# Kernel tuning notes

Measured on AMD Instinct MI355X. Metric: run time of the kernel, lower is better.

The kernel has to match this reference:

```python
import jax, jax.numpy as jnp
import numpy as np

GROUP = 16          # c.MAX_GROUP_SIZE
NEG_SLOPE = 0.2     # GATConv default negative_slope
BN_EPS = 1e-5       # BatchNorm1d eps (eval mode, running stats (0,1))


def setup_inputs() -> dict:
    key = jax.random.key(0)
    ks = iter(jax.random.split(key, 64))
    N, E, F_IN = 8192, 262144, 1024
    d = {}
    d['x'] = jax.random.normal(next(ks), (N, F_IN), jnp.float32)
    d['edge_index'] = jax.random.randint(next(ks), (2, E), 0, N, dtype=jnp.int32)
    def p(shape, scale=0.05):
        return jax.random.normal(next(ks), shape, jnp.float32) * scale
    # GATConv params (heads=1): lin weight [in,out] (no bias), att_src/att_dst [out], bias [out]
    d['W1'], d['a1s'], d['a1d'], d['b1'] = p((F_IN, 128)), p((128,)), p((128,)), p((128,))
    d['W2'], d['a2s'], d['a2d'], d['b2'] = p((128, 256)), p((256,)), p((256,)), p((256,))
    d['W3'], d['a3s'], d['a3d'], d['b3'] = p((256, 128)), p((128,)), p((128,)), p((128,))
    # LSTM: 2 layers, bidirectional, hidden=128 -> gates 4*128=512. PyTorch layout [4H,in],[4H,H]
    for l, in_sz in [(0, 128), (1, 256)]:
        for sfx in ['', 'r']:
            d['Wih%d%s' % (l, sfx)] = p((512, in_sz))
            d['Whh%d%s' % (l, sfx)] = p((512, 128))
            d['bih%d%s' % (l, sfx)] = p((512,))
            d['bhh%d%s' % (l, sfx)] = p((512,))
    # MLP head (torch Linear weight [out,in]) + BatchNorm affine params
    d['fc1w'], d['fc1b'] = p((256, 256)), p((256,))
    d['g1'], d['be1'] = jnp.ones((256,), jnp.float32), jnp.zeros((256,), jnp.float32)
    d['fc2w'], d['fc2b'] = p((64, 256)), p((64,))
    d['g2'], d['be2'] = jnp.ones((64,), jnp.float32), jnp.zeros((64,), jnp.float32)
    d['fc3w'], d['fc3b'] = p((3, 64)), p((3,))
    return d


def _segment_softmax(e, dst, n):
    m = jax.ops.segment_max(e, dst, num_segments=n)
    ex = jnp.exp(e - m[dst])
    s = jax.ops.segment_sum(ex, dst, num_segments=n)
    return ex / (s[dst] + 1e-16)  # PyG softmax adds 1e-16


def _gat_conv(x, src, dst, W, a_s, a_d, b, n):
    h = x @ W                                   # [N, F]
    e = (h * a_s).sum(-1)[src] + (h * a_d).sum(-1)[dst]
    e = jnp.where(e >= 0, e, NEG_SLOPE * e)      # leaky_relu
    alpha = _segment_softmax(e, dst, n)          # [E]
    out = jax.ops.segment_sum(alpha[:, None] * h[src], dst, num_segments=n)
    return out + b, alpha


def _lstm_dir(x, Wih, Whh, bih, bhh, reverse):
    H = Whh.shape[1]
    xp = x @ Wih.T + bih + bhh                   # precompute input projections [L,4H]
    def step(carry, xt):
        h, c = carry
        g = xt + h @ Whh.T
        i, f, gg, o = jnp.split(g, 4)
        i, f, o = jax.nn.sigmoid(i), jax.nn.sigmoid(f), jax.nn.sigmoid(o)
        c = f * c + i * jnp.tanh(gg)
        h = o * jnp.tanh(c)
        return (h, c), h
    init = (jnp.zeros((H,), x.dtype), jnp.zeros((H,), x.dtype))
    _, hs = jax.lax.scan(step, init, xp, reverse=reverse)
    return hs  # [L,H], index-aligned with input


def _bn_eval(z, g, b):
    # BatchNorm1d eval with running_mean=0, running_var=1
    return z * (g / jnp.sqrt(1.0 + BN_EPS)) + b


def reference(x, edge_index, W1, a1s, a1d, b1, W2, a2s, a2d, b2, W3, a3s, a3d, b3,
              Wih0, Whh0, bih0, bhh0, Wih0r, Whh0r, bih0r, bhh0r,
              Wih1, Whh1, bih1, bhh1, Wih1r, Whh1r, bih1r, bhh1r,
              fc1w, fc1b, g1, be1, fc2w, fc2b, g2, be2, fc3w, fc3b):
    N = x.shape[0]
    loops = jnp.arange(N, dtype=edge_index.dtype)   # GATConv adds self-loops
    src = jnp.concatenate([edge_index[0], loops])
    dst = jnp.concatenate([edge_index[1], loops])

    h, a1 = _gat_conv(x, src, dst, W1, a1s, a1d, b1, N)
    h = jax.nn.relu(h)                               # dropout is no-op in eval
    h, a2 = _gat_conv(h, src, dst, W2, a2s, a2d, b2, N)
    h = jax.nn.relu(h)
    h, a3 = _gat_conv(h, src, dst, W3, a3s, a3d, b3, N)
    h = jax.nn.relu(h)

    # 2-layer bidirectional LSTM over the node sequence (unbatched, as in torch)
    y = jnp.concatenate([_lstm_dir(h, Wih0, Whh0, bih0, bhh0, False),
                         _lstm_dir(h, Wih0r, Whh0r, bih0r, bhh0r, True)], axis=-1)
    y = jnp.concatenate([_lstm_dir(y, Wih1, Whh1, bih1, bhh1, False),
                         _lstm_dir(y, Wih1r, Whh1r, bih1r, bhh1r, True)], axis=-1)

    # global_mean_pool with batch = arange(B).repeat_interleave(GROUP)
    pooled = y.reshape(-1, GROUP, y.shape[-1]).mean(axis=1)   # [B, 256]

    z = jax.nn.relu(pooled @ fc1w.T + fc1b)
    z = _bn_eval(z, g1, be1)
    z = jax.nn.relu(z @ fc2w.T + fc2b)
    z = _bn_eval(z, g2, be2)
    logits = z @ fc3w.T + fc3b                       # [B, 3]
    return (logits, a1, a2, a3, jnp.stack([src, dst]))
```

## Files before the change

### kernel.cpp

```cpp
#include <hip/hip_runtime.h>

#define N_NODES 8192
#define E_EDGES 262144
#define ET (E_EDGES + N_NODES)

#define O_A1 1536
#define O_A2 (O_A1 + ET)
#define O_A3 (O_A2 + ET)
#define O_SD (O_A3 + ET)

#define CHUNK 32
#define WARM  32
#define NCHUNK 256

typedef float f32x4 __attribute__((ext_vector_type(4)));
typedef int   int4v __attribute__((ext_vector_type(4)));
typedef _Float16 half8 __attribute__((ext_vector_type(8)));
typedef _Float16 half4 __attribute__((ext_vector_type(4)));

#define LDS_BARRIER() asm volatile("s_waitcnt lgkmcnt(0)\n\ts_barrier" ::: "memory")

static __device__ __forceinline__ float fast_tanh(float x) {
    float e = __builtin_amdgcn_exp2f(-2.88539008f * x);
    return 2.0f * __builtin_amdgcn_rcpf(1.0f + e) - 1.0f;
}
static __device__ __forceinline__ f32x4 cvt4(half4 h) {
    f32x4 v;
    v[0] = (float)h[0]; v[1] = (float)h[1]; v[2] = (float)h[2]; v[3] = (float)h[3];
    return v;
}

__global__ __launch_bounds__(256) void k_edges(const int* __restrict__ ei,
                                               int* __restrict__ src_i, int* __restrict__ dst_i,
                                               float* __restrict__ out_sd, int* __restrict__ counts) {
    int i = blockIdx.x * 256 + threadIdx.x;
    if (i >= ET) return;
    int s, d;
    if (i < E_EDGES) { s = ei[i]; d = ei[E_EDGES + i]; }
    else { s = d = i - E_EDGES; }
    src_i[i] = s; dst_i[i] = d;
    out_sd[i] = (float)s;
    out_sd[ET + i] = (float)d;
    atomicAdd(&counts[d], 1);
}

__global__ __launch_bounds__(1024) void k_scan(const int* __restrict__ counts,
                                               int* __restrict__ rowptr, int* __restrict__ cursor) {
    __shared__ int part[1024];
    const int tid = threadIdx.x;
    const int base = tid * 8;
    int loc[8]; int run = 0;
#pragma unroll
    for (int i = 0; i < 8; ++i) { loc[i] = run; run += counts[base + i]; }
    part[tid] = run;
    __syncthreads();
    for (int off = 1; off < 1024; off <<= 1) {
        int v = (tid >= off) ? part[tid - off] : 0;
        __syncthreads();
        part[tid] += v;
        __syncthreads();
    }
    int pre = tid ? part[tid - 1] : 0;
#pragma unroll
    for (int i = 0; i < 8; ++i) {
        int v = pre + loc[i];
        rowptr[base + i] = v;
        cursor[base + i] = v;
    }
    if (tid == 1023) rowptr[N_NODES] = part[1023];
}

__global__ __launch_bounds__(256) void k_scatter(const int* __restrict__ dst_i,
                                                 int* __restrict__ cursor, int* __restrict__ esort) {
    int i = blockIdx.x * 256 + threadIdx.x;
    if (i >= ET) return;
    int pos = atomicAdd(&cursor[dst_i[i]], 1);
    esort[pos] = i;
}

__global__ __launch_bounds__(256) void k_cvt_t(const float* __restrict__ B, _Float16* __restrict__ Bt,
                                               int K, int N) {
    __shared__ float tile[32][33];
    const int k0 = blockIdx.x * 32, n0 = blockIdx.y * 32;
    const int tx = threadIdx.x & 31, ty = threadIdx.x >> 5;
#pragma unroll
    for (int i = 0; i < 32; i += 8)
        tile[ty + i][tx] = B[(size_t)(k0 + ty + i) * N + n0 + tx];
    __syncthreads();
#pragma unroll
    for (int i = 0; i < 32; i += 8)
        Bt[(size_t)(n0 + ty + i) * K + k0 + tx] = (_Float16)tile[tx][ty + i];
}

__global__ __launch_bounds__(256) void k_cvt(const float* __restrict__ B, _Float16* __restrict__ Bt,
                                             int total) {
    int i = (blockIdx.x * 256 + threadIdx.x) * 4;
    if (i >= total) return;
    float4 v = *(const float4*)(B + i);
    half4 h;
    h[0] = (_Float16)v.x; h[1] = (_Float16)v.y; h[2] = (_Float16)v.z; h[3] = (_Float16)v.w;
    *(half4*)(Bt + i) = h;
}

__global__ __launch_bounds__(512) void k_qwhh(const float* __restrict__ Wa, const float* __restrict__ Wb,
                                              const float* __restrict__ Wc, const float* __restrict__ Wd,
                                              int4v* __restrict__ wq_all, float* __restrict__ sc_all) {
    const int mat = blockIdx.x;
    const float* __restrict__ Whh = mat == 0 ? Wa : mat == 1 ? Wb : mat == 2 ? Wc : Wd;
    const int tid = threadIdx.x;
    const int w = tid >> 6, lane = tid & 63, col = lane & 15, quad = lane >> 4;
    const int grow0 = (col & 3) * 128 + w * 16 + (col >> 2);
    int4v* outp = wq_all + ((size_t)mat * 512 + tid) * 8;
#pragma unroll
    for (int mt = 0; mt < 4; ++mt) {
        const float* wr = Whh + (size_t)(grow0 + mt * 4) * 128;
        float wf[32];
        float amax = 0.f;
#pragma unroll
        for (int kc = 0; kc < 2; ++kc)
#pragma unroll
            for (int j = 0; j < 16; ++j) {
                float v = wr[kc * 64 + quad * 16 + j];
                wf[kc * 16 + j] = v;
                amax = fmaxf(amax, fabsf(v));
            }
        amax = fmaxf(amax, __shfl_xor(amax, 16));
        amax = fmaxf(amax, __shfl_xor(amax, 32));
        float qs = 127.0f / amax;
#pragma unroll
        for (int kc = 0; kc < 2; ++kc) {
            int4v v;
#pragma unroll
            for (int d = 0; d < 4; ++d) {
                int word = 0;
#pragma unroll
                for (int b = 0; b < 4; ++b) {
                    int q = (int)__builtin_rintf(wf[kc * 16 + d * 4 + b] * qs);
                    word |= (q & 255) << (8 * b);
                }
                v[d] = word;
            }
            outp[mt * 2 + kc] = v;
        }
        if (quad == 0) sc_all[(size_t)mat * 512 + grow0 + mt * 4] = -1.44269504f * amax * (1.0f / 16129.0f);
    }
}

__global__ __launch_bounds__(256) void gemm_mfma(const float* __restrict__ A, const _Float16* __restrict__ Bt,
                                                 float* __restrict__ C, _Float16* __restrict__ C16,
                                                 int M, int N, int K,
                                                 const float* __restrict__ b1, const float* __restrict__ b2,
                                                 int perm) {
    __shared__ __align__(16) _Float16 As[64][40];
    __shared__ __align__(16) _Float16 Bs[64][40];
    const int tid = threadIdx.x;
    const int w = tid >> 6, lane = tid & 63, col = lane & 15, quad = lane >> 4;
    const int m0 = blockIdx.x * 64, n0 = blockIdx.y * 64;
    const int sm = tid >> 2;
    const int sk = (tid & 3) * 8;
    const f32x4 zf = {0.f, 0.f, 0.f, 0.f};
    f32x4 acc[4] = {zf, zf, zf, zf};

    const float* ap = A + (size_t)(m0 + sm) * K + sk;
    const _Float16* bp = Bt + (size_t)(n0 + sm) * K + sk;

    for (int k0 = 0; k0 < K; k0 += 32) {
        float4 a01 = *(const float4*)(ap + k0);
        float4 a23 = *(const float4*)(ap + k0 + 4);
        half8 af;
        af[0] = (_Float16)a01.x; af[1] = (_Float16)a01.y;
        af[2] = (_Float16)a01.z; af[3] = (_Float16)a01.w;
        af[4] = (_Float16)a23.x; af[5] = (_Float16)a23.y;
        af[6] = (_Float16)a23.z; af[7] = (_Float16)a23.w;
        *(half8*)(&As[sm][sk]) = af;
        *(half8*)(&Bs[sm][sk]) = *(const half8*)(bp + k0);
        __syncthreads();
        half8 afr = *(const half8*)(&As[w * 16 + col][quad * 8]);
#pragma unroll
        for (int nt = 0; nt < 4; ++nt) {
            half8 bfr = *(const half8*)(&Bs[nt * 16 + col][quad * 8]);
            acc[nt] = __builtin_amdgcn_mfma_f32_16x16x32_f16(afr, bfr, acc[nt], 0, 0, 0);
        }
        __syncthreads();
    }
#pragma unroll
    for (int nt = 0; nt < 4; ++nt) {
        const int n = n0 + nt * 16 + col;
        float bias = 0.f;
        if (b1) bias += b1[n];
        if (b2) bias += b2[n];
        if (perm) {
            const int he = n & 127, type = n >> 7;
            const int nout = he * 4 + type;
#pragma unroll
            for (int r = 0; r < 4; ++r) {
                const int m = m0 + w * 16 + quad * 4 + r;
                C16[(size_t)m * N + nout] = (_Float16)((acc[nt][r] + bias) * -1.44269504f);
            }
        } else {
#pragma unroll
            for (int r = 0; r < 4; ++r) {
                const int m = m0 + w * 16 + quad * 4 + r;
                float v = acc[nt][r] + bias;
                C[(size_t)m * N + n] = v;
                if (C16) C16[(size_t)m * N + n] = (_Float16)v;
            }
        }
    }
}

__global__ __launch_bounds__(256) void gemm_tn(const float* __restrict__ A, const float* __restrict__ B,
                                               float* __restrict__ C, int M, int N, int K,
                                               const float* __restrict__ b1,
                                               int do_relu, const float* __restrict__ bng,
                                               const float* __restrict__ bnb) {
    __shared__ __align__(16) float As[16][68];
    __shared__ __align__(16) float Bs[16][68];
    const int tid = threadIdx.x;
    const int tx = tid & 15, ty = tid >> 4;
    const int m0 = blockIdx.x * 64, n0 = blockIdx.y * 64;
    float acc[4][4] = {};
    for (int k0 = 0; k0 < K; k0 += 16) {
        const int ar = tid >> 4, ac = tid & 15;
#pragma unroll
        for (int i = 0; i < 4; ++i)
            As[ac][ar + i * 16] = A[(size_t)(m0 + ar + i * 16) * K + k0 + ac];
#pragma unroll
        for (int i = 0; i < 4; ++i) {
            int n = n0 + (tid >> 4) + i * 16;
            Bs[tid & 15][(tid >> 4) + i * 16] = (n < N) ? B[(size_t)n * K + k0 + (tid & 15)] : 0.f;
        }
        __syncthreads();
#pragma unroll
        for (int kk = 0; kk < 16; ++kk) {
            float4 a4 = *(const float4*)&As[kk][ty * 4];
            float4 b4 = *(const float4*)&Bs[kk][tx * 4];
            float av[4] = {a4.x, a4.y, a4.z, a4.w};
            float bv[4] = {b4.x, b4.y, b4.z, b4.w};
#pragma unroll
            for (int i = 0; i < 4; ++i)
#pragma unroll
                for (int j = 0; j < 4; ++j) acc[i][j] = fmaf(av[i], bv[j], acc[i][j]);
        }
        __syncthreads();
    }
#pragma unroll
    for (int i = 0; i < 4; ++i)
#pragma unroll
        for (int j = 0; j < 4; ++j) {
            int n = n0 + tx * 4 + j;
            if (n >= N) continue;
            float v = acc[i][j];
            if (b1) v += b1[n];
            if (do_relu) v = fmaxf(v, 0.f);
            if (bng) v = v * (bng[n] * rsqrtf(1.f + 1e-5f)) + bnb[n];
            C[(size_t)(m0 + ty * 4 + i) * N + n] = v;
        }
}

__global__ __launch_bounds__(256) void attn_scores(const float* __restrict__ h,
                                                   const float* __restrict__ a_s, const float* __restrict__ a_d,
                                                   float* __restrict__ ssrc, float* __restrict__ sdst, int F) {
    const int wave = threadIdx.x >> 6, lane = threadIdx.x & 63;
    const int n = blockIdx.x * 4 + wave;
    const float* hr = h + (size_t)n * F;
    float va = 0.f, vd = 0.f;
    for (int f = lane; f < F; f += 64) { float hv = hr[f]; va += hv * a_s[f]; vd += hv * a_d[f]; }
    for (int o = 32; o; o >>= 1) { va += __shfl_down(va, o); vd += __shfl_down(vd, o); }
    if (lane == 0) { ssrc[n] = va; sdst[n] = vd; }
}

__global__ __launch_bounds__(256) void gat_agg(const _Float16* __restrict__ h16,
                                               const float* __restrict__ ssrc, const float* __restrict__ sdst,
                                               const int* __restrict__ rowptr, const int* __restrict__ esort,
                                               const int* __restrict__ src_i, const float* __restrict__ bias,
                                               float* __restrict__ outh, float* __restrict__ alpha_out, int F) {
    const int n = blockIdx.x, tid = threadIdx.x;
    const int r0 = rowptr[n], r1 = rowptr[n + 1];
    const int deg = r1 - r0;
    const float sd = sdst[n];
    __shared__ float redA[4], redB[4];
    float m = -1e30f;
    for (int j = tid; j < deg; j += 256) {
        int eid = esort[r0 + j];
        float e = ssrc[src_i[eid]] + sd;
        e = (e >= 0.f) ? e : 0.2f * e;
        m = fmaxf(m, e);
    }
    for (int o = 32; o; o >>= 1) m = fmaxf(m, __shfl_down(m, o));
    if ((tid & 63) == 0) redA[tid >> 6] = m;
    __syncthreads();
    m = fmaxf(fmaxf(redA[0], redA[1]), fmaxf(redA[2], redA[3]));
    float s = 0.f;
    for (int j = tid; j < deg; j += 256) {
        int eid = esort[r0 + j];
        float e = ssrc[src_i[eid]] + sd;
        e = (e >= 0.f) ? e : 0.2f * e;
        s += __expf(e - m);
    }
    for (int o = 32; o; o >>= 1) s += __shfl_down(s, o);
    if ((tid & 63) == 0) redB[tid >> 6] = s;
    __syncthreads();
    s = redB[0] + redB[1] + redB[2] + redB[3];
    const float inv = 1.f / (s + 1e-16f);

    __shared__ float la[256];
    __shared__ int ls[256];
    __shared__ float red[2048];
    const int sh = (F == 128) ? 4 : 5;
    const int ES = 256 >> sh;
    const int slot = tid >> sh;
    const int fg = (tid & ((1 << sh) - 1)) * 8;
    float acc[8] = {};
    for (int base = 0; base < deg; base += 256) {
        __syncthreads();
        int j = base + tid;
        if (j < deg) {
            int eid = esort[r0 + j];
            int sidx = src_i[eid];
            float e = ssrc[sidx] + sd;
            e = (e >= 0.f) ? e : 0.2f * e;
            float al = __expf(e - m) * inv;
            la[tid] = al; ls[tid] = sidx;
            alpha_out[eid] = al;
        }
        __syncthreads();
        int cnt = min(256, deg - base);
        for (int jj = slot; jj < cnt; jj += ES) {
            float al = la[jj];
            half8 hv = *(const half8*)(h16 + (size_t)ls[jj] * F + fg);
#pragma unroll
            for (int k = 0; k < 8; ++k) acc[k] = fmaf(al, (float)hv[k], acc[k]);
        }
    }
    __syncthreads();
#pragma unroll
    for (int k = 0; k < 8; k += 4) {
        f32x4 v = {acc[k], acc[k + 1], acc[k + 2], acc[k + 3]};
        *(f32x4*)(red + slot * F + fg + k) = v;
    }
    __syncthreads();
    if (tid < F) {
        float a = 0.f;
        for (int sN = 0; sN < ES; ++sN) a += red[sN * F + tid];
        outh[(size_t)n * F + tid] = fmaxf(a + bias[tid], 0.f);
    }
}

__global__ __launch_bounds__(512) void lstm_mfma(const _Float16* __restrict__ xpF, const _Float16* __restrict__ xpB,
                                                 const int4v* __restrict__ wq_all, const float* __restrict__ sc_all,
                                                 float* __restrict__ y, int T) {
    const int blk = blockIdx.x;
    const int dir = blk >> 8;
    const int cj  = blk & 255;
    const _Float16* __restrict__ xp = dir ? xpB : xpF;
    const int tid  = threadIdx.x;
    const int w    = tid >> 6;
    const int lane = tid & 63;
    const int col  = lane & 15;
    const int quad = lane >> 4;

    __shared__ float sc_lds[512];
    __shared__ char  h8[2][128];

    int4v wq[4][2];
    const int4v* wqp = wq_all + ((size_t)dir * 512 + tid) * 8;
#pragma unroll
    for (int mt = 0; mt < 4; ++mt)
#pragma unroll
        for (int kc = 0; kc < 2; ++kc)
            wq[mt][kc] = wqp[mt * 2 + kc];
    sc_lds[tid] = sc_all[dir * 512 + tid];
    if (tid < 128) { h8[0][tid] = 0; h8[1][tid] = 0; }
    float c = 0.f;

    const int he = w * 16 + (col & 3) * 4 + quad;
    LDS_BARRIER();
    const float sc0 = sc_lds[he], sc1 = sc_lds[128 + he],
                sc2 = sc_lds[256 + he], sc3 = sc_lds[384 + he];

    const int warm = dir == 0 ? (cj ? WARM : 0) : (cj == NCHUNK - 1 ? 0 : WARM);
    const int t_start = dir == 0 ? (cj * CHUNK - warm)
                                 : (cj * CHUNK + CHUNK - 1 + warm);

    const ptrdiff_t step1  = dir ? -512 : 512;
    const ptrdiff_t dstep4 = 4 * step1;
    const ptrdiff_t ystep  = dir ? -256 : 256;
    const _Float16* xbase = xp + he * 4;
    const _Float16* p0 = xbase + (ptrdiff_t)t_start * 512;
    const _Float16* p1 = p0 + step1;
    const _Float16* p2 = p1 + step1;
    const _Float16* p3 = p2 + step1;
    float* py = y + (ptrdiff_t)t_start * 256 + dir * 128;

    f32x4 r0 = cvt4(*(const half4*)p0);
    f32x4 r1 = cvt4(*(const half4*)p1);
    f32x4 r2 = cvt4(*(const half4*)p2);
    f32x4 r3 = cvt4(*(const half4*)p3);

#define LSTM_STEP(RS, PS, PB, DO_REFILL, DO_WRITE) do { \
        const char* hsrc_ = h8[PB]; \
        int4v hq0 = *(const int4v*)(hsrc_ + quad * 16); \
        int4v hq1 = *(const int4v*)(hsrc_ + 64 + quad * 16); \
        f32x4 xq = RS; \
        int4v z4 = {0, 0, 0, 0}; \
        int4v a0 = __builtin_amdgcn_mfma_i32_16x16x64_i8(wq[0][0], hq0, z4, 0, 0, 0); \
        int4v a1 = __builtin_amdgcn_mfma_i32_16x16x64_i8(wq[1][0], hq0, z4, 0, 0, 0); \
        int4v a2 = __builtin_amdgcn_mfma_i32_16x16x64_i8(wq[2][0], hq0, z4, 0, 0, 0); \
        int4v a3 = __builtin_amdgcn_mfma_i32_16x16x64_i8(wq[3][0], hq0, z4, 0, 0, 0); \
        if (DO_REFILL) { PS += dstep4; RS = cvt4(*(const half4*)(PS)); } \
        a0 = __builtin_amdgcn_mfma_i32_16x16x64_i8(wq[0][1], hq1, a0, 0, 0, 0); \
        a1 = __builtin_amdgcn_mfma_i32_16x16x64_i8(wq[1][1], hq1, a1, 0, 0, 0); \
        a2 = __builtin_amdgcn_mfma_i32_16x16x64_i8(wq[2][1], hq1, a2, 0, 0, 0); \
        a3 = __builtin_amdgcn_mfma_i32_16x16x64_i8(wq[3][1], hq1, a3, 0, 0, 0); \
        int4v g4 = (col == 0) ? a0 : (col == 1) ? a1 : (col == 2) ? a2 : a3; \
        float gi = fmaf((float)g4[0], sc0, xq[0]); \
        float gf = fmaf((float)g4[1], sc1, xq[1]); \
        float gg = fmaf((float)g4[2], sc2, xq[2]); \
        float go = fmaf((float)g4[3], sc3, xq[3]); \
        float i_ = __builtin_amdgcn_rcpf(1.0f + __builtin_amdgcn_exp2f(gi)); \
        float f_ = __builtin_amdgcn_rcpf(1.0f + __builtin_amdgcn_exp2f(gf)); \
        float o_ = __builtin_amdgcn_rcpf(1.0f + __builtin_amdgcn_exp2f(go)); \
        float tg = fmaf(2.0f, __builtin_amdgcn_rcpf(1.0f + __builtin_amdgcn_exp2f(gg + gg)), -1.0f); \
        c = fmaf(f_, c, i_ * tg); \
        float hh = o_ * fast_tanh(c); \
        if (col < 4) { \
            h8[1 - (PB)][he] = (char)(int)__builtin_rintf(hh * 127.0f); \
            if (DO_WRITE) py[he] = hh; \
        } \
        py += ystep; \
        LDS_BARRIER(); \
    } while (0)

    for (int g = 0; g < warm; g += 4) {
        LSTM_STEP(r0, p0, 0, 1, 0);
        LSTM_STEP(r1, p1, 1, 1, 0);
        LSTM_STEP(r2, p2, 0, 1, 0);
        LSTM_STEP(r3, p3, 1, 1, 0);
    }
    for (int g = 0; g < CHUNK - 4; g += 4) {
        LSTM_STEP(r0, p0, 0, 1, 1);
        LSTM_STEP(r1, p1, 1, 1, 1);
        LSTM_STEP(r2, p2, 0, 1, 1);
        LSTM_STEP(r3, p3, 1, 1, 1);
    }
    LSTM_STEP(r0, p0, 0, 0, 1);
    LSTM_STEP(r1, p1, 1, 0, 1);
    LSTM_STEP(r2, p2, 0, 0, 1);
    LSTM_STEP(r3, p3, 1, 0, 1);
#undef LSTM_STEP
}

__global__ __launch_bounds__(256) void k_pool(const float* __restrict__ y, float* __restrict__ pooled) {
    const int b = blockIdx.x, f = threadIdx.x;
    float s = 0.f;
#pragma unroll
    for (int g = 0; g < 16; ++g) s += y[((size_t)b * 16 + g) * 256 + f];
    pooled[b * 256 + f] = s * (1.f / 16.f);
}

extern "C" void kernel_launch(void* const* d_in, const int* in_sizes, int n_in,
                              void* d_out, int out_size, void* d_ws, size_t ws_size,
                              hipStream_t stream) {
    const float* x    = (const float*)d_in[0];
    const int*   ei   = (const int*)d_in[1];
    const float* W1   = (const float*)d_in[2];
    const float* a1s  = (const float*)d_in[3];
    const float* a1d  = (const float*)d_in[4];
    const float* b1   = (const float*)d_in[5];
    const float* W2   = (const float*)d_in[6];
    const float* a2s  = (const float*)d_in[7];
    const float* a2d  = (const float*)d_in[8];
    const float* b2   = (const float*)d_in[9];
    const float* W3   = (const float*)d_in[10];
    const float* a3s  = (const float*)d_in[11];
    const float* a3d  = (const float*)d_in[12];
    const float* b3   = (const float*)d_in[13];
    const float* Wih0 = (const float*)d_in[14];
    const float* Whh0 = (const float*)d_in[15];
    const float* bih0 = (const float*)d_in[16];
    const float* bhh0 = (const float*)d_in[17];
    const float* Wih0r= (const float*)d_in[18];
    const float* Whh0r= (const float*)d_in[19];
    const float* bih0r= (const float*)d_in[20];
    const float* bhh0r= (const float*)d_in[21];
    const float* Wih1 = (const float*)d_in[22];
    const float* Whh1 = (const float*)d_in[23];
    const float* bih1 = (const float*)d_in[24];
    const float* bhh1 = (const float*)d_in[25];
    const float* Wih1r= (const float*)d_in[26];
    const float* Whh1r= (const float*)d_in[27];
    const float* bih1r= (const float*)d_in[28];
    const float* bhh1r= (const float*)d_in[29];
    const float* fc1w = (const float*)d_in[30];
    const float* fc1b = (const float*)d_in[31];
    const float* g1   = (const float*)d_in[32];
    const float* be1  = (const float*)d_in[33];
    const float* fc2w = (const float*)d_in[34];
    const float* fc2b = (const float*)d_in[35];
    const float* g2   = (const float*)d_in[36];
    const float* be2  = (const float*)d_in[37];
    const float* fc3w = (const float*)d_in[38];
    const float* fc3b = (const float*)d_in[39];
    float* out = (float*)d_out;

    char* p = (char*)d_ws;
    auto alloc = [&](size_t bytes) -> void* {
        void* r = (void*)p;
        p += (bytes + 255) & ~(size_t)255;
        return r;
    };
    int* src_i   = (int*)alloc((size_t)ET * 4);
    int* dst_i   = (int*)alloc((size_t)ET * 4);
    int* counts  = (int*)alloc((size_t)N_NODES * 4);
    int* rowptr  = (int*)alloc((size_t)(N_NODES + 1) * 4);
    int* cursor  = (int*)alloc((size_t)N_NODES * 4);
    int* esort   = (int*)alloc((size_t)ET * 4);
    float* hbuf  = (float*)alloc((size_t)N_NODES * 256 * 4);
    float* bufA  = (float*)alloc((size_t)N_NODES * 256 * 4);
    float* bufB  = (float*)alloc((size_t)N_NODES * 256 * 4);
    _Float16* h16 = (_Float16*)alloc((size_t)N_NODES * 256 * 2);
    float* ssrc  = (float*)alloc((size_t)N_NODES * 4);
    float* sdst  = (float*)alloc((size_t)N_NODES * 4);
    _Float16* xpF = (_Float16*)alloc((size_t)N_NODES * 512 * 2);
    _Float16* xpB = (_Float16*)alloc((size_t)N_NODES * 512 * 2);
    float* pooled= (float*)alloc((size_t)512 * 256 * 4);
    float* z1    = (float*)alloc((size_t)512 * 256 * 4);
    float* z2    = (float*)alloc((size_t)512 * 64 * 4);
    _Float16* Bt1 = (_Float16*)alloc((size_t)128 * 1024 * 2);
    _Float16* Bt2 = (_Float16*)alloc((size_t)256 * 128 * 2);
    _Float16* Bt3 = (_Float16*)alloc((size_t)128 * 256 * 2);
    _Float16* Wt0 = (_Float16*)alloc((size_t)512 * 128 * 2);
    _Float16* Wt0r= (_Float16*)alloc((size_t)512 * 128 * 2);
    _Float16* Wt1 = (_Float16*)alloc((size_t)512 * 256 * 2);
    _Float16* Wt1r= (_Float16*)alloc((size_t)512 * 256 * 2);
    int4v* wq_all = (int4v*)alloc((size_t)4 * 512 * 8 * 16);
    float* sc_all = (float*)alloc((size_t)4 * 512 * 4);

    k_cvt_t<<<dim3(32, 4), 256, 0, stream>>>(W1, Bt1, 1024, 128);
    k_cvt_t<<<dim3(4, 8), 256, 0, stream>>>(W2, Bt2, 128, 256);
    k_cvt_t<<<dim3(8, 4), 256, 0, stream>>>(W3, Bt3, 256, 128);
    k_cvt<<<64, 256, 0, stream>>>(Wih0,  Wt0,  512 * 128);
    k_cvt<<<64, 256, 0, stream>>>(Wih0r, Wt0r, 512 * 128);
    k_cvt<<<128, 256, 0, stream>>>(Wih1,  Wt1,  512 * 256);
    k_cvt<<<128, 256, 0, stream>>>(Wih1r, Wt1r, 512 * 256);
    k_qwhh<<<4, 512, 0, stream>>>(Whh0, Whh0r, Whh1, Whh1r, wq_all, sc_all);

    const int EB = (ET + 255) / 256;
    hipMemsetAsync(counts, 0, (size_t)N_NODES * 4, stream);
    k_edges<<<EB, 256, 0, stream>>>(ei, src_i, dst_i, out + O_SD, counts);
    k_scan<<<1, 1024, 0, stream>>>(counts, rowptr, cursor);
    k_scatter<<<EB, 256, 0, stream>>>(dst_i, cursor, esort);

    gemm_mfma<<<dim3(128, 2), 256, 0, stream>>>(x, Bt1, hbuf, h16, N_NODES, 128, 1024, nullptr, nullptr, 0);
    attn_scores<<<N_NODES / 4, 256, 0, stream>>>(hbuf, a1s, a1d, ssrc, sdst, 128);
    gat_agg<<<N_NODES, 256, 0, stream>>>(h16, ssrc, sdst, rowptr, esort, src_i, b1, bufA, out + O_A1, 128);

    gemm_mfma<<<dim3(128, 4), 256, 0, stream>>>(bufA, Bt2, hbuf, h16, N_NODES, 256, 128, nullptr, nullptr, 0);
    attn_scores<<<N_NODES / 4, 256, 0, stream>>>(hbuf, a2s, a2d, ssrc, sdst, 256);
    gat_agg<<<N_NODES, 256, 0, stream>>>(h16, ssrc, sdst, rowptr, esort, src_i, b2, bufB, out + O_A2, 256);

    gemm_mfma<<<dim3(128, 2), 256, 0, stream>>>(bufB, Bt3, hbuf, h16, N_NODES, 128, 256, nullptr, nullptr, 0);
    attn_scores<<<N_NODES / 4, 256, 0, stream>>>(hbuf, a3s, a3d, ssrc, sdst, 128);
    gat_agg<<<N_NODES, 256, 0, stream>>>(h16, ssrc, sdst, rowptr, esort, src_i, b3, bufA, out + O_A3, 128);

    gemm_mfma<<<dim3(128, 8), 256, 0, stream>>>(bufA, Wt0,  nullptr, xpF, N_NODES, 512, 128, bih0,  bhh0,  1);
    gemm_mfma<<<dim3(128, 8), 256, 0, stream>>>(bufA, Wt0r, nullptr, xpB, N_NODES, 512, 128, bih0r, bhh0r, 1);
    lstm_mfma<<<2 * NCHUNK, 512, 0, stream>>>(xpF, xpB, wq_all, sc_all, bufB, N_NODES);

    gemm_mfma<<<dim3(128, 8), 256, 0, stream>>>(bufB, Wt1,  nullptr, xpF, N_NODES, 512, 256, bih1,  bhh1,  1);
    gemm_mfma<<<dim3(128, 8), 256, 0, stream>>>(bufB, Wt1r, nullptr, xpB, N_NODES, 512, 256, bih1r, bhh1r, 1);
    lstm_mfma<<<2 * NCHUNK, 512, 0, stream>>>(xpF, xpB, wq_all + (size_t)2 * 512 * 8, sc_all + 2 * 512, hbuf, N_NODES);

    k_pool<<<512, 256, 0, stream>>>(hbuf, pooled);
    gemm_tn<<<dim3(8, 4), 256, 0, stream>>>(pooled, fc1w, z1, 512, 256, 256, fc1b, 1, g1, be1);
    gemm_tn<<<dim3(8, 1), 256, 0, stream>>>(z1, fc2w, z2, 512, 64, 256, fc2b, 1, g2, be2);
    gemm_tn<<<dim3(8, 1), 256, 0, stream>>>(z2, fc3w, out, 512, 3, 64, fc3b, 0, nullptr, nullptr);
}
```

Before: 564.1 us.

## Double-buffer GEMM LDS, single-pass GAT softmax, fp16 scores, merge conversion kernels

The MFMA GEMM now double-buffers its LDS tiles and prefetches the next K slice into registers, so each iteration needs one barrier instead of two. GAT aggregation computes max, sum and alpha in a single pass when a node's degree fits in one block, which avoids re-reading edge indices and scores three times. Attention scores now read the fp16 h copy, so the fp32 GEMM output store is dropped. The seven weight-conversion launches are merged into two. In exchange the GEMM uses twice the LDS, and the scores are computed from fp16-rounded features, which slightly changes precision.

```diff
diff --git a/kernel.cpp b/kernel.cpp
--- a/kernel.cpp
+++ b/kernel.cpp
@@ -78,10 +78,35 @@
     esort[pos] = i;
 }
 
-__global__ __launch_bounds__(256) void k_cvt_t(const float* __restrict__ B, _Float16* __restrict__ Bt,
-                                               int K, int N) {
+__global__ __launch_bounds__(256) void k_cvt_all(const float* __restrict__ Wa, const float* __restrict__ Wb,
+                                                 const float* __restrict__ Wc, const float* __restrict__ Wd,
+                                                 _Float16* __restrict__ Ta, _Float16* __restrict__ Tb,
+                                                 _Float16* __restrict__ Tc, _Float16* __restrict__ Td) {
+    int b = blockIdx.x;
+    const float* src; _Float16* dst; int base;
+    if (b < 64) { src = Wa; dst = Ta; base = b; }
+    else if (b < 128) { src = Wb; dst = Tb; base = b - 64; }
+    else if (b < 256) { src = Wc; dst = Tc; base = b - 128; }
+    else { src = Wd; dst = Td; base = b - 256; }
+    int i = (base * 256 + threadIdx.x) * 4;
+    float4 v = *(const float4*)(src + i);
+    half4 h;
+    h[0] = (_Float16)v.x; h[1] = (_Float16)v.y; h[2] = (_Float16)v.z; h[3] = (_Float16)v.w;
+    *(half4*)(dst + i) = h;
+}
+
+__global__ __launch_bounds__(256) void k_cvt_t_all(const float* __restrict__ W1, const float* __restrict__ W2,
+                                                   const float* __restrict__ W3,
+                                                   _Float16* __restrict__ B1, _Float16* __restrict__ B2,
+                                                   _Float16* __restrict__ B3) {
     __shared__ float tile[32][33];
-    const int k0 = blockIdx.x * 32, n0 = blockIdx.y * 32;
+    int b = blockIdx.x;
+    const float* B; _Float16* Bt; int K, N, kb;
+    if (b < 128) { B = W1; Bt = B1; K = 1024; N = 128; kb = b; }
+    else if (b < 160) { B = W2; Bt = B2; K = 128; N = 256; kb = b - 128; }
+    else { B = W3; Bt = B3; K = 256; N = 128; kb = b - 160; }
+    const int ktiles = K >> 5;
+    const int k0 = (kb % ktiles) * 32, n0 = (kb / ktiles) * 32;
     const int tx = threadIdx.x & 31, ty = threadIdx.x >> 5;
 #pragma unroll
     for (int i = 0; i < 32; i += 8)
@@ -90,16 +115,6 @@
 #pragma unroll
     for (int i = 0; i < 32; i += 8)
         Bt[(size_t)(n0 + ty + i) * K + k0 + tx] = (_Float16)tile[tx][ty + i];
-}
-
-__global__ __launch_bounds__(256) void k_cvt(const float* __restrict__ B, _Float16* __restrict__ Bt,
-                                             int total) {
-    int i = (blockIdx.x * 256 + threadIdx.x) * 4;
-    if (i >= total) return;
-    float4 v = *(const float4*)(B + i);
-    half4 h;
-    h[0] = (_Float16)v.x; h[1] = (_Float16)v.y; h[2] = (_Float16)v.z; h[3] = (_Float16)v.w;
-    *(half4*)(Bt + i) = h;
 }
 
 __global__ __launch_bounds__(512) void k_qwhh(const float* __restrict__ Wa, const float* __restrict__ Wb,
@@ -151,8 +166,8 @@
                                                  int M, int N, int K,
                                                  const float* __restrict__ b1, const float* __restrict__ b2,
                                                  int perm) {
-    __shared__ __align__(16) _Float16 As[64][40];
-    __shared__ __align__(16) _Float16 Bs[64][40];
+    __shared__ __align__(16) _Float16 As[2][64][40];
+    __shared__ __align__(16) _Float16 Bs[2][64][40];
     const int tid = threadIdx.x;
     const int w = tid >> 6, lane = tid & 63, col = lane & 15, quad = lane >> 4;
     const int m0 = blockIdx.x * 64, n0 = blockIdx.y * 64;
@@ -164,24 +179,45 @@
     const float* ap = A + (size_t)(m0 + sm) * K + sk;
     const _Float16* bp = Bt + (size_t)(n0 + sm) * K + sk;
 
-    for (int k0 = 0; k0 < K; k0 += 32) {
-        float4 a01 = *(const float4*)(ap + k0);
-        float4 a23 = *(const float4*)(ap + k0 + 4);
+    {
+        float4 a01 = *(const float4*)ap;
+        float4 a23 = *(const float4*)(ap + 4);
         half8 af;
         af[0] = (_Float16)a01.x; af[1] = (_Float16)a01.y;
         af[2] = (_Float16)a01.z; af[3] = (_Float16)a01.w;
         af[4] = (_Float16)a23.x; af[5] = (_Float16)a23.y;
         af[6] = (_Float16)a23.z; af[7] = (_Float16)a23.w;
-        *(half8*)(&As[sm][sk]) = af;
-        *(half8*)(&Bs[sm][sk]) = *(const half8*)(bp + k0);
-        __syncthreads();
-        half8 afr = *(const half8*)(&As[w * 16 + col][quad * 8]);
+        *(half8*)(&As[0][sm][sk]) = af;
+        *(half8*)(&Bs[0][sm][sk]) = *(const half8*)bp;
+    }
+    __syncthreads();
+
+    const int nk = K >> 5;
+    for (int ki = 0; ki < nk; ++ki) {
+        const int cur = ki & 1;
+        float4 a01n, a23n; half8 bfn;
+        const bool more = (ki + 1 < nk);
+        if (more) {
+            a01n = *(const float4*)(ap + (ki + 1) * 32);
+            a23n = *(const float4*)(ap + (ki + 1) * 32 + 4);
+            bfn  = *(const half8*)(bp + (ki + 1) * 32);
+        }
+        half8 afr = *(const half8*)(&As[cur][w * 16 + col][quad * 8]);
 #pragma unroll
         for (int nt = 0; nt < 4; ++nt) {
-            half8 bfr = *(const half8*)(&Bs[nt * 16 + col][quad * 8]);
+            half8 bfr = *(const half8*)(&Bs[cur][nt * 16 + col][quad * 8]);
             acc[nt] = __builtin_amdgcn_mfma_f32_16x16x32_f16(afr, bfr, acc[nt], 0, 0, 0);
         }
-        __syncthreads();
+        if (more) {
+            half8 af;
+            af[0] = (_Float16)a01n.x; af[1] = (_Float16)a01n.y;
+            af[2] = (_Float16)a01n.z; af[3] = (_Float16)a01n.w;
+            af[4] = (_Float16)a23n.x; af[5] = (_Float16)a23n.y;
+            af[6] = (_Float16)a23n.z; af[7] = (_Float16)a23n.w;
+            *(half8*)(&As[cur ^ 1][sm][sk]) = af;
+            *(half8*)(&Bs[cur ^ 1][sm][sk]) = bfn;
+            __syncthreads();
+        }
     }
 #pragma unroll
     for (int nt = 0; nt < 4; ++nt) {
@@ -202,7 +238,7 @@
             for (int r = 0; r < 4; ++r) {
                 const int m = m0 + w * 16 + quad * 4 + r;
                 float v = acc[nt][r] + bias;
-                C[(size_t)m * N + n] = v;
+                if (C)   C[(size_t)m * N + n] = v;
                 if (C16) C16[(size_t)m * N + n] = (_Float16)v;
             }
         }
@@ -258,14 +294,14 @@
         }
 }
 
-__global__ __launch_bounds__(256) void attn_scores(const float* __restrict__ h,
+__global__ __launch_bounds__(256) void attn_scores(const _Float16* __restrict__ h,
                                                    const float* __restrict__ a_s, const float* __restrict__ a_d,
                                                    float* __restrict__ ssrc, float* __restrict__ sdst, int F) {
     const int wave = threadIdx.x >> 6, lane = threadIdx.x & 63;
     const int n = blockIdx.x * 4 + wave;
-    const float* hr = h + (size_t)n * F;
+    const _Float16* hr = h + (size_t)n * F;
     float va = 0.f, vd = 0.f;
-    for (int f = lane; f < F; f += 64) { float hv = hr[f]; va += hv * a_s[f]; vd += hv * a_d[f]; }
+    for (int f = lane; f < F; f += 64) { float hv = (float)hr[f]; va += hv * a_s[f]; vd += hv * a_d[f]; }
     for (int o = 32; o; o >>= 1) { va += __shfl_down(va, o); vd += __shfl_down(vd, o); }
     if (lane == 0) { ssrc[n] = va; sdst[n] = vd; }
 }
@@ -280,30 +316,6 @@
     const int deg = r1 - r0;
     const float sd = sdst[n];
     __shared__ float redA[4], redB[4];
-    float m = -1e30f;
-    for (int j = tid; j < deg; j += 256) {
-        int eid = esort[r0 + j];
-        float e = ssrc[src_i[eid]] + sd;
-        e = (e >= 0.f) ? e : 0.2f * e;
-        m = fmaxf(m, e);
-    }
-    for (int o = 32; o; o >>= 1) m = fmaxf(m, __shfl_down(m, o));
-    if ((tid & 63) == 0) redA[tid >> 6] = m;
-    __syncthreads();
-    m = fmaxf(fmaxf(redA[0], redA[1]), fmaxf(redA[2], redA[3]));
-    float s = 0.f;
-    for (int j = tid; j < deg; j += 256) {
-        int eid = esort[r0 + j];
-        float e = ssrc[src_i[eid]] + sd;
-        e = (e >= 0.f) ? e : 0.2f * e;
-        s += __expf(e - m);
-    }
-    for (int o = 32; o; o >>= 1) s += __shfl_down(s, o);
-    if ((tid & 63) == 0) redB[tid >> 6] = s;
-    __syncthreads();
-    s = redB[0] + redB[1] + redB[2] + redB[3];
-    const float inv = 1.f / (s + 1e-16f);
-
     __shared__ float la[256];
     __shared__ int ls[256];
     __shared__ float red[2048];
@@ -312,25 +324,85 @@
     const int slot = tid >> sh;
     const int fg = (tid & ((1 << sh) - 1)) * 8;
     float acc[8] = {};
-    for (int base = 0; base < deg; base += 256) {
-        __syncthreads();
-        int j = base + tid;
-        if (j < deg) {
-            int eid = esort[r0 + j];
-            int sidx = src_i[eid];
-            float e = ssrc[sidx] + sd;
+
+    if (deg <= 256) {
+        int eid = 0, sidx = 0;
+        float e = -1e30f;
+        if (tid < deg) {
+            eid = esort[r0 + tid];
+            sidx = src_i[eid];
+            e = ssrc[sidx] + sd;
             e = (e >= 0.f) ? e : 0.2f * e;
-            float al = __expf(e - m) * inv;
-            la[tid] = al; ls[tid] = sidx;
+        }
+        float m = e;
+        for (int o = 32; o; o >>= 1) m = fmaxf(m, __shfl_down(m, o));
+        if ((tid & 63) == 0) redA[tid >> 6] = m;
+        __syncthreads();
+        m = fmaxf(fmaxf(redA[0], redA[1]), fmaxf(redA[2], redA[3]));
+        float ex = (tid < deg) ? __expf(e - m) : 0.f;
+        float s = ex;
+        for (int o = 32; o; o >>= 1) s += __shfl_down(s, o);
+        if ((tid & 63) == 0) redB[tid >> 6] = s;
+        __syncthreads();
+        s = redB[0] + redB[1] + redB[2] + redB[3];
+        const float inv = 1.f / (s + 1e-16f);
+        if (tid < deg) {
+            float al = ex * inv;
             alpha_out[eid] = al;
-        }
-        __syncthreads();
-        int cnt = min(256, deg - base);
-        for (int jj = slot; jj < cnt; jj += ES) {
+            la[tid] = al;
+            ls[tid] = sidx;
+        }
+        __syncthreads();
+        for (int jj = slot; jj < deg; jj += ES) {
             float al = la[jj];
             half8 hv = *(const half8*)(h16 + (size_t)ls[jj] * F + fg);
 #pragma unroll
             for (int k = 0; k < 8; ++k) acc[k] = fmaf(al, (float)hv[k], acc[k]);
+        }
+    } else {
+        float m = -1e30f;
+        for (int j = tid; j < deg; j += 256) {
+            int eid = esort[r0 + j];
+            float e = ssrc[src_i[eid]] + sd;
+            e = (e >= 0.f) ? e : 0.2f * e;
+            m = fmaxf(m, e);
+        }
+        for (int o = 32; o; o >>= 1) m = fmaxf(m, __shfl_down(m, o));
+        if ((tid & 63) == 0) redA[tid >> 6] = m;
+        __syncthreads();
+        m = fmaxf(fmaxf(redA[0], redA[1]), fmaxf(redA[2], redA[3]));
+        float s = 0.f;
+        for (int j = tid; j < deg; j += 256) {
+            int eid = esort[r0 + j];
+            float e = ssrc[src_i[eid]] + sd;
+            e = (e >= 0.f) ? e : 0.2f * e;
+            s += __expf(e - m);
+        }
+        for (int o = 32; o; o >>= 1) s += __shfl_down(s, o);
+        if ((tid & 63) == 0) redB[tid >> 6] = s;
+        __syncthreads();
+        s = redB[0] + redB[1] + redB[2] + redB[3];
+        const float inv = 1.f / (s + 1e-16f);
+        for (int base = 0; base < deg; base += 256) {
+            __syncthreads();
+            int j = base + tid;
+            if (j < deg) {
+                int eid = esort[r0 + j];
+                int sidx = src_i[eid];
+                float e = ssrc[sidx] + sd;
+                e = (e >= 0.f) ? e : 0.2f * e;
+                float al = __expf(e - m) * inv;
+                la[tid] = al; ls[tid] = sidx;
+                alpha_out[eid] = al;
+            }
+            __syncthreads();
+            int cnt = min(256, deg - base);
+            for (int jj = slot; jj < cnt; jj += ES) {
+                float al = la[jj];
+                half8 hv = *(const half8*)(h16 + (size_t)ls[jj] * F + fg);
+#pragma unroll
+                for (int k = 0; k < 8; ++k) acc[k] = fmaf(al, (float)hv[k], acc[k]);
+            }
         }
     }
     __syncthreads();
@@ -537,13 +609,8 @@
     int4v* wq_all = (int4v*)alloc((size_t)4 * 512 * 8 * 16);
     float* sc_all = (float*)alloc((size_t)4 * 512 * 4);
 
-    k_cvt_t<<<dim3(32, 4), 256, 0, stream>>>(W1, Bt1, 1024, 128);
-    k_cvt_t<<<dim3(4, 8), 256, 0, stream>>>(W2, Bt2, 128, 256);
-    k_cvt_t<<<dim3(8, 4), 256, 0, stream>>>(W3, Bt3, 256, 128);
-    k_cvt<<<64, 256, 0, stream>>>(Wih0,  Wt0,  512 * 128);
-    k_cvt<<<64, 256, 0, stream>>>(Wih0r, Wt0r, 512 * 128);
-    k_cvt<<<128, 256, 0, stream>>>(Wih1,  Wt1,  512 * 256);
-    k_cvt<<<128, 256, 0, stream>>>(Wih1r, Wt1r, 512 * 256);
+    k_cvt_t_all<<<192, 256, 0, stream>>>(W1, W2, W3, Bt1, Bt2, Bt3);
+    k_cvt_all<<<384, 256, 0, stream>>>(Wih0, Wih0r, Wih1, Wih1r, Wt0, Wt0r, Wt1, Wt1r);
     k_qwhh<<<4, 512, 0, stream>>>(Whh0, Whh0r, Whh1, Whh1r, wq_all, sc_all);
 
     const int EB = (ET + 255) / 256;
@@ -552,16 +619,16 @@
     k_scan<<<1, 1024, 0, stream>>>(counts, rowptr, cursor);
     k_scatter<<<EB, 256, 0, stream>>>(dst_i, cursor, esort);
 
-    gemm_mfma<<<dim3(128, 2), 256, 0, stream>>>(x, Bt1, hbuf, h16, N_NODES, 128, 1024, nullptr, nullptr, 0);
-    attn_scores<<<N_NODES / 4, 256, 0, stream>>>(hbuf, a1s, a1d, ssrc, sdst, 128);
+    gemm_mfma<<<dim3(128, 2), 256, 0, stream>>>(x, Bt1, nullptr, h16, N_NODES, 128, 1024, nullptr, nullptr, 0);
+    attn_scores<<<N_NODES / 4, 256, 0, stream>>>(h16, a1s, a1d, ssrc, sdst, 128);
     gat_agg<<<N_NODES, 256, 0, stream>>>(h16, ssrc, sdst, rowptr, esort, src_i, b1, bufA, out + O_A1, 128);
 
-    gemm_mfma<<<dim3(128, 4), 256, 0, stream>>>(bufA, Bt2, hbuf, h16, N_NODES, 256, 128, nullptr, nullptr, 0);
-    attn_scores<<<N_NODES / 4, 256, 0, stream>>>(hbuf, a2s, a2d, ssrc, sdst, 256);
+    gemm_mfma<<<dim3(128, 4), 256, 0, stream>>>(bufA, Bt2, nullptr, h16, N_NODES, 256, 128, nullptr, nullptr, 0);
+    attn_scores<<<N_NODES / 4, 256, 0, stream>>>(h16, a2s, a2d, ssrc, sdst, 256);
     gat_agg<<<N_NODES, 256, 0, stream>>>(h16, ssrc, sdst, rowptr, esort, src_i, b2, bufB, out + O_A2, 256);
 
-    gemm_mfma<<<dim3(128, 2), 256, 0, stream>>>(bufB, Bt3, hbuf, h16, N_NODES, 128, 256, nullptr, nullptr, 0);
-    attn_scores<<<N_NODES / 4, 256, 0, stream>>>(hbuf, a3s, a3d, ssrc, sdst, 128);
+    gemm_mfma<<<dim3(128, 2), 256, 0, stream>>>(bufB, Bt3, nullptr, h16, N_NODES, 128, 256, nullptr, nullptr, 0);
+    attn_scores<<<N_NODES / 4, 256, 0, stream>>>(h16, a3s, a3d, ssrc, sdst, 128);
     gat_agg<<<N_NODES, 256, 0, stream>>>(h16, ssrc, sdst, rowptr, esort, src_i, b3, bufA, out + O_A3, 128);
 
     gemm_mfma<<<dim3(128, 8), 256, 0, stream>>>(bufA, Wt0,  nullptr, xpF, N_NODES, 512, 128, bih0,  bhh0,  1);
```

New measurement: 531.5 us. 1.06x faster.
